# Optimization experiments

Hardware: AMD Instinct MI355X
Metric: run time of the kernel (lower is better)

The kernel has to match this reference:

```python
import jax, jax.numpy as jnp
import numpy as np


def swiglu(g, u):
    return jax.nn.silu(g) * u


def setup_inputs() -> dict:
    key = jax.random.key(0)
    ks = jax.random.split(key, 10)
    D, H, E, HS = 2048, 512, 32, 1024
    B, S = 1, 2048
    s = 0.02
    return {
        "x": jax.random.normal(ks[0], (B, S, D), jnp.float32),
        "gate_w": jax.random.normal(ks[1], (E, D), jnp.float32) * s,
        "expert_bias": jnp.zeros((E,), jnp.float32),
        "wg": jax.random.normal(ks[2], (E, D, H), jnp.float32) * s,
        "wu": jax.random.normal(ks[3], (E, D, H), jnp.float32) * s,
        "wd": jax.random.normal(ks[4], (E, H, D), jnp.float32) * s,
        "sg": jax.random.normal(ks[5], (D, HS), jnp.float32) * s,
        "su": jax.random.normal(ks[6], (D, HS), jnp.float32) * s,
        "sd": jax.random.normal(ks[7], (HS, D), jnp.float32) * s,
        "coef_w": jax.random.normal(ks[8], (2, D), jnp.float32) * s,
        "coef_b": jnp.zeros((2,), jnp.float32),
        "top_k": 4,
    }


def reference(x, gate_w, expert_bias, wg, wu, wd, sg, su, sd, coef_w, coef_b, top_k):
    # --- sigmoid router with bias-adjusted top-k selection ---
    logits = jnp.einsum("bsd,ed->bse", x, gate_w)            # [B,S,E]
    routing = jax.nn.sigmoid(logits.astype(jnp.float32))
    biased = routing + expert_bias[None, None, :]
    _, inds = jax.lax.top_k(biased, top_k)                    # [B,S,k]
    scores = jnp.take_along_axis(routing, inds, axis=-1)      # gather UNbiased weights
    scores = scores / (jnp.sum(scores, axis=-1, keepdims=True) + 1e-20)  # norm_topk_prob
    scores = scores.astype(x.dtype)

    # --- SwitchGLU experts: dense per-expert SwiGLU, then gather top-k outputs ---
    h = jnp.einsum("bsd,edh->bseh", x, wg)                    # [B,S,E,H]
    u = jnp.einsum("bsd,edh->bseh", x, wu)
    y_all = jnp.einsum("bseh,ehd->bsed", swiglu(h, u), wd)    # [B,S,E,D]
    expert_out = jnp.take_along_axis(
        y_all, inds[..., None], axis=2)                        # [B,S,k,D]
    y_experts = jnp.sum(expert_out * scores[..., None], axis=-2)  # [B,S,D]

    # --- shared expert + learned 2-way mixing coefficient ---
    shared = swiglu(x @ sg, x @ su) @ sd                      # [B,S,D]
    coef = jax.nn.softmax(jnp.einsum("bsd,cd->bsc", x, coef_w) + coef_b, axis=-1)
    return y_experts * coef[..., :1] + shared * coef[..., 1:]
```

## Files before the change

kernel.cpp:

```cpp
#include <hip/hip_runtime.h>
#include <hip/hip_bf16.h>
#include <stdint.h>

#define S_TOK   2048
#define DMODEL  2048
#define HEXP    512
#define NEXP    32
#define HSH     1024
#define NPAIR   (S_TOK * 4)
#define NT128   96
#define NT64    160

#define M128_NT  0
#define M128_TE  1
#define M128_TP0 (1 + NT128)
#define M128_TM  (1 + 2 * NT128)
#define M64_NT   (1 + 3 * NT128)
#define M64_TE   (M64_NT + 1)
#define M64_TP0  (M64_NT + 1 + NT64)
#define M64_TM   (M64_NT + 1 + 2 * NT64)
#define META_SIZE (M64_NT + 1 + 3 * NT64)

typedef short  s16x8 __attribute__((ext_vector_type(8)));
typedef __bf16 b16x8 __attribute__((ext_vector_type(8)));
typedef float  f32x4 __attribute__((ext_vector_type(4)));

__device__ __forceinline__ f32x4 mfma16x16x32(s16x8 a, s16x8 b, f32x4 c) {
    return __builtin_amdgcn_mfma_f32_16x16x32_bf16(
        __builtin_bit_cast(b16x8, a), __builtin_bit_cast(b16x8, b), c, 0, 0, 0);
}

__device__ __forceinline__ unsigned short f2bf(float f) {
    union { float f; unsigned int u; } v; v.f = f;
    unsigned int u = v.u;
    return (unsigned short)((u + 0x7FFFu + ((u >> 16) & 1u)) >> 16);
}

__device__ __forceinline__ float bf2f(unsigned short b) {
    union { unsigned int u; float f; } v; v.u = ((unsigned int)b) << 16;
    return v.f;
}

__device__ __forceinline__ void gload16(const unsigned short* g, unsigned short* l) {
    __builtin_amdgcn_global_load_lds(
        (const __attribute__((address_space(1))) void*)(uintptr_t)g,
        (__attribute__((address_space(3))) void*)(uintptr_t)l, 16, 0, 0);
}

__device__ __forceinline__ int src_col8(int lane) {
    return 8 * ((lane & 3) ^ ((lane >> 3) & 3));
}
__device__ __forceinline__ int frag_ko(int fr, int fq) {
    return 8 * (fq ^ ((fr >> 1) & 3));
}

__device__ __forceinline__ void tconv_tile(const float* __restrict__ s,
                                           unsigned short* __restrict__ d,
                                           const int K, const int N,
                                           const int k0, const int n0,
                                           unsigned short* pool)
{
    auto T = (unsigned short (*)[80])pool;
    const int tid = threadIdx.x;
    const int n4 = (tid & 15) * 4;
    const int kr = tid >> 4;
#pragma unroll
    for (int i = 0; i < 4; ++i) {
        const int k = kr + i * 16;
        const float4 v = *reinterpret_cast<const float4*>(s + (size_t)(k0 + k) * N + n0 + n4);
        T[n4 + 0][k] = f2bf(v.x);
        T[n4 + 1][k] = f2bf(v.y);
        T[n4 + 2][k] = f2bf(v.z);
        T[n4 + 3][k] = f2bf(v.w);
    }
    __syncthreads();
    const int nw = tid >> 2;
    const int kc = (tid & 3) * 16;
    uint4* o = reinterpret_cast<uint4*>(d + (size_t)(n0 + nw) * K + k0 + kc);
    o[0] = *reinterpret_cast<const uint4*>(&T[nw][kc]);
    o[1] = *reinterpret_cast<const uint4*>(&T[nw][kc + 8]);
}

__global__ __launch_bounds__(256)
void router_kernel(const float* __restrict__ x, const float* __restrict__ gate_w,
                   const float* __restrict__ expert_bias,
                   const float* __restrict__ coef_w, const float* __restrict__ coef_b,
                   int* __restrict__ inds, float* __restrict__ scores,
                   float* __restrict__ coefo)
{
    const int t = blockIdx.x;
    const int tid = threadIdx.x;
    const int lane = tid & 63;
    const int wave = tid >> 6;
    const float* xr = x + (size_t)t * DMODEL;

    float xv[32];
#pragma unroll
    for (int j = 0; j < 32; ++j) xv[j] = xr[lane + 64 * j];

    __shared__ float s_logits[NEXP];
    __shared__ float s_coef[2];

    for (int i = 0; i < 8; ++i) {
        const int e = wave * 8 + i;
        const float* wr = gate_w + (size_t)e * DMODEL;
        float p = 0.f;
#pragma unroll
        for (int j = 0; j < 32; ++j) p += xv[j] * wr[lane + 64 * j];
#pragma unroll
        for (int o = 32; o > 0; o >>= 1) p += __shfl_xor(p, o);
        if (lane == 0) s_logits[e] = p;
    }
    if (wave == 0) {
        for (int c = 0; c < 2; ++c) {
            const float* wr = coef_w + (size_t)c * DMODEL;
            float p = 0.f;
#pragma unroll
            for (int j = 0; j < 32; ++j) p += xv[j] * wr[lane + 64 * j];
#pragma unroll
            for (int o = 32; o > 0; o >>= 1) p += __shfl_xor(p, o);
            if (lane == 0) s_coef[c] = p;
        }
    }
    __syncthreads();
    if (tid == 0) {
        float routing[NEXP], biased[NEXP];
        for (int e = 0; e < NEXP; ++e) {
            const float r = 1.f / (1.f + expf(-s_logits[e]));
            routing[e] = r;
            biased[e] = r + expert_bias[e];
        }
        int sel[4]; float sc[4]; float ssum = 0.f;
        for (int k = 0; k < 4; ++k) {
            int best = 0; float bv = -1e30f;
            for (int e = 0; e < NEXP; ++e)
                if (biased[e] > bv) { bv = biased[e]; best = e; }
            sel[k] = best; sc[k] = routing[best]; ssum += sc[k];
            biased[best] = -1e30f;
        }
        const float inv = 1.f / (ssum + 1e-20f);
        for (int k = 0; k < 4; ++k) {
            inds[t * 4 + k] = sel[k];
            scores[t * 4 + k] = sc[k] * inv;
        }
        const float l0 = s_coef[0] + coef_b[0];
        const float l1 = s_coef[1] + coef_b[1];
        const float m = fmaxf(l0, l1);
        const float e0 = expf(l0 - m), e1 = expf(l1 - m);
        coefo[t * 2 + 0] = e0 / (e0 + e1);
        coefo[t * 2 + 1] = e1 / (e0 + e1);
    }
}

__global__ __launch_bounds__(256)
void xcast_kernel(const float* __restrict__ x, unsigned short* __restrict__ xb)
{
    const int i = (blockIdx.x * 256 + threadIdx.x) * 4;
    const float4 v = *reinterpret_cast<const float4*>(x + i);
    ushort4 o;
    o.x = f2bf(v.x); o.y = f2bf(v.y); o.z = f2bf(v.z); o.w = f2bf(v.w);
    *reinterpret_cast<ushort4*>(xb + i) = o;
}

__global__ __launch_bounds__(256)
void tconv_kernel(const float* __restrict__ src, unsigned short* __restrict__ dst,
                  const int K, const int N)
{
    __shared__ unsigned short pool[64 * 80];
    const size_t boff = (size_t)blockIdx.z * K * N;
    tconv_tile(src + boff, dst + boff, K, N, blockIdx.y * 64, blockIdx.x * 64, pool);
}

__global__ __launch_bounds__(1024)
void group_kernel(const int* __restrict__ inds, const float* __restrict__ scores,
                  int* __restrict__ meta, int* __restrict__ pair_token,
                  float* __restrict__ pair_score, int* __restrict__ tok_pos)
{
    __shared__ int cnt[NEXP];
    __shared__ int off_s[NEXP];
    __shared__ int cur[NEXP];
    const int tid = threadIdx.x;
    if (tid < NEXP) cnt[tid] = 0;
    __syncthreads();
    for (int i = tid; i < NPAIR; i += 1024) atomicAdd(&cnt[inds[i]], 1);
    __syncthreads();
    if (tid == 0) {
        int run = 0, nt1 = 0, nt2 = 0;
        for (int e = 0; e < NEXP; ++e) {
            off_s[e] = run;
            const int c = cnt[e];
            for (int m0 = 0; m0 < c; m0 += 128) {
                meta[M128_TE + nt1] = e;
                meta[M128_TP0 + nt1] = run + m0;
                meta[M128_TM + nt1] = (c - m0 < 128) ? (c - m0) : 128;
                ++nt1;
            }
            for (int m0 = 0; m0 < c; m0 += 64) {
                meta[M64_TE + nt2] = e;
                meta[M64_TP0 + nt2] = run + m0;
                meta[M64_TM + nt2] = (c - m0 < 64) ? (c - m0) : 64;
                ++nt2;
            }
            run += c;
        }
        meta[M128_NT] = nt1;
        meta[M64_NT] = nt2;
    }
    __syncthreads();
    if (tid < NEXP) cur[tid] = off_s[tid];
    __syncthreads();
    for (int i = tid; i < NPAIR; i += 1024) {
        const int e = inds[i];
        const int pos = atomicAdd(&cur[e], 1);
        pair_token[pos] = i >> 2;
        pair_score[pos] = scores[i];
        tok_pos[i] = pos;
    }
}

__global__ __launch_bounds__(256, 4)
void gateup_e_kernel(const unsigned short* __restrict__ xb,
                     const unsigned short* __restrict__ Bg_all,
                     const unsigned short* __restrict__ Bu_all,
                     unsigned short* __restrict__ act,
                     const int* __restrict__ meta, const int* __restrict__ pair_token,
                     const float* __restrict__ sg, const float* __restrict__ su,
                     const float* __restrict__ sd,
                     unsigned short* __restrict__ sgb, unsigned short* __restrict__ sub_,
                     unsigned short* __restrict__ sdb)
{
    constexpr int NT = DMODEL / 32;
    constexpr int NB = HEXP;
    __shared__ unsigned short pool[16384];
    auto Al  = (unsigned short (*)[128][32])(pool);
    auto Bgl = (unsigned short (*)[64][32])(pool + 8192);
    auto Bul = (unsigned short (*)[64][32])(pool + 12288);

    const int tid = threadIdx.x;
    const int lane = tid & 63;
    const int wave = tid >> 6;

    if (blockIdx.y >= NT128) {
        const int tile = (blockIdx.y - NT128) * 8 + blockIdx.x;
        const int which = tile / 512;
        const int t = tile % 512;
        if (which == 0)      tconv_tile(sg, sgb, DMODEL, HSH, (t >> 4) * 64, (t & 15) * 64, pool);
        else if (which == 1) tconv_tile(su, sub_, DMODEL, HSH, (t >> 4) * 64, (t & 15) * 64, pool);
        else                 tconv_tile(sd, sdb, HSH, DMODEL, (t >> 5) * 64, (t & 31) * 64, pool);
        return;
    }

    const int tt = blockIdx.y;
    if (tt >= meta[M128_NT]) return;
    const int e = meta[M128_TE + tt];
    const int p0 = meta[M128_TP0 + tt];
    const int mval = meta[M128_TM + tt];
    const size_t eoff = (size_t)e * NB * DMODEL;
    const unsigned short* Bg = Bg_all + eoff;
    const unsigned short* Bu = Bu_all + eoff;
    const int n0 = blockIdx.x * 64;

    const int sub  = lane >> 2;
    const int col8 = src_col8(lane);
    const int arow0 = wave * 32 + sub;
    const int arow1 = arow0 + 16;
    int q0 = p0 + arow0; if (q0 > NPAIR - 1) q0 = NPAIR - 1;
    int q1 = p0 + arow1; if (q1 > NPAIR - 1) q1 = NPAIR - 1;
    const int tok0 = pair_token[q0];
    const int tok1 = pair_token[q1];
    const unsigned short* asrc0 = xb + (size_t)tok0 * DMODEL + col8;
    const unsigned short* asrc1 = xb + (size_t)tok1 * DMODEL + col8;
    const int brow = wave * 16 + sub;
    const unsigned short* gsrc = Bg + (size_t)(n0 + brow) * DMODEL + col8;
    const unsigned short* usrc = Bu + (size_t)(n0 + brow) * DMODEL + col8;

    auto stage = [&](int buf, int k0) {
        gload16(asrc0 + k0, &Al[buf][wave * 32][0]);
        gload16(asrc1 + k0, &Al[buf][wave * 32 + 16][0]);
        gload16(gsrc + k0, &Bgl[buf][wave * 16][0]);
        gload16(usrc + k0, &Bul[buf][wave * 16][0]);
    };

    const int wm = wave >> 1, wn = wave & 1;
    const int fr = lane & 15, fq = lane >> 4;
    const int ko = frag_ko(fr, fq);

    const f32x4 zero4 = {0.f, 0.f, 0.f, 0.f};
    f32x4 hacc[4][2], uacc[4][2];
#pragma unroll
    for (int m = 0; m < 4; ++m)
#pragma unroll
        for (int n = 0; n < 2; ++n) { hacc[m][n] = zero4; uacc[m][n] = zero4; }

    auto compute = [&](int buf) {
        s16x8 af[4], bg[2], bu[2];
#pragma unroll
        for (int m = 0; m < 4; ++m)
            af[m] = *reinterpret_cast<const s16x8*>(&Al[buf][wm * 64 + m * 16 + fr][ko]);
#pragma unroll
        for (int n = 0; n < 2; ++n) {
            bg[n] = *reinterpret_cast<const s16x8*>(&Bgl[buf][wn * 32 + n * 16 + fr][ko]);
            bu[n] = *reinterpret_cast<const s16x8*>(&Bul[buf][wn * 32 + n * 16 + fr][ko]);
        }
#pragma unroll
        for (int m = 0; m < 4; ++m)
#pragma unroll
            for (int n = 0; n < 2; ++n) {
                hacc[m][n] = mfma16x16x32(af[m], bg[n], hacc[m][n]);
                uacc[m][n] = mfma16x16x32(af[m], bu[n], uacc[m][n]);
            }
    };

    stage(0, 0);
    __syncthreads();
#pragma unroll 1
    for (int t = 0; t < NT; ++t) {
        const int cur = t & 1;
        if (t + 1 < NT) stage(cur ^ 1, (t + 1) * 32);
        compute(cur);
        __syncthreads();
    }

#pragma unroll
    for (int m = 0; m < 4; ++m)
#pragma unroll
        for (int n = 0; n < 2; ++n) {
            const int col = n0 + wn * 32 + n * 16 + fr;
#pragma unroll
            for (int r = 0; r < 4; ++r) {
                const int rt = wm * 64 + m * 16 + fq * 4 + r;
                if (rt < mval) {
                    const float hv = hacc[m][n][r];
                    const float a = hv / (1.f + __expf(-hv)) * uacc[m][n][r];
                    act[(size_t)(p0 + rt) * NB + col] = f2bf(a);
                }
            }
        }
}

__global__ __launch_bounds__(256, 4)
void gateup_s_kernel(const unsigned short* __restrict__ xb,
                     const unsigned short* __restrict__ Bg,
                     const unsigned short* __restrict__ Bu,
                     unsigned short* __restrict__ act,
                     const float* __restrict__ wd, unsigned short* __restrict__ wdb)
{
    constexpr int NT = DMODEL / 32;
    constexpr int NB = HSH;
    __shared__ unsigned short pool[12288];
    auto Al  = (unsigned short (*)[64][32])(pool);
    auto Bgl = (unsigned short (*)[64][32])(pool + 4096);
    auto Bul = (unsigned short (*)[64][32])(pool + 8192);

    const int tid = threadIdx.x;
    const int lane = tid & 63;
    const int wave = tid >> 6;

    if (blockIdx.y >= S_TOK / 64) {
        const int tile = (blockIdx.y - S_TOK / 64) * 16 + blockIdx.x;
        const int e = tile >> 8;
        const int t = tile & 255;
        tconv_tile(wd + (size_t)e * HEXP * DMODEL, wdb + (size_t)e * DMODEL * HEXP,
                   HEXP, DMODEL, (t >> 5) * 64, (t & 31) * 64, pool);
        return;
    }

    const int p0 = blockIdx.y * 64;
    const int n0 = blockIdx.x * 64;

    const int sub  = lane >> 2;
    const int col8 = src_col8(lane);
    const int arow = wave * 16 + sub;
    const unsigned short* asrc = xb + (size_t)(p0 + arow) * DMODEL + col8;
    const unsigned short* gsrc = Bg + (size_t)(n0 + arow) * DMODEL + col8;
    const unsigned short* usrc = Bu + (size_t)(n0 + arow) * DMODEL + col8;

    auto stage = [&](int buf, int k0) {
        gload16(asrc + k0, &Al[buf][wave * 16][0]);
        gload16(gsrc + k0, &Bgl[buf][wave * 16][0]);
        gload16(usrc + k0, &Bul[buf][wave * 16][0]);
    };

    const int wm = wave >> 1, wn = wave & 1;
    const int fr = lane & 15, fq = lane >> 4;
    const int ko = frag_ko(fr, fq);

    const f32x4 zero4 = {0.f, 0.f, 0.f, 0.f};
    f32x4 hacc[2][2], uacc[2][2];
#pragma unroll
    for (int m = 0; m < 2; ++m)
#pragma unroll
        for (int n = 0; n < 2; ++n) { hacc[m][n] = zero4; uacc[m][n] = zero4; }

    auto compute = [&](int buf) {
        s16x8 af[2], bg[2], bu[2];
#pragma unroll
        for (int m = 0; m < 2; ++m)
            af[m] = *reinterpret_cast<const s16x8*>(&Al[buf][wm * 32 + m * 16 + fr][ko]);
#pragma unroll
        for (int n = 0; n < 2; ++n) {
            bg[n] = *reinterpret_cast<const s16x8*>(&Bgl[buf][wn * 32 + n * 16 + fr][ko]);
            bu[n] = *reinterpret_cast<const s16x8*>(&Bul[buf][wn * 32 + n * 16 + fr][ko]);
        }
#pragma unroll
        for (int m = 0; m < 2; ++m)
#pragma unroll
            for (int n = 0; n < 2; ++n) {
                hacc[m][n] = mfma16x16x32(af[m], bg[n], hacc[m][n]);
                uacc[m][n] = mfma16x16x32(af[m], bu[n], uacc[m][n]);
            }
    };

    stage(0, 0);
    __syncthreads();
#pragma unroll 1
    for (int t = 0; t < NT; ++t) {
        const int cur = t & 1;
        if (t + 1 < NT) stage(cur ^ 1, (t + 1) * 32);
        compute(cur);
        __syncthreads();
    }

#pragma unroll
    for (int m = 0; m < 2; ++m)
#pragma unroll
        for (int n = 0; n < 2; ++n) {
            const int col = n0 + wn * 32 + n * 16 + fr;
#pragma unroll
            for (int r = 0; r < 4; ++r) {
                const int rt = wm * 32 + m * 16 + fq * 4 + r;
                const float hv = hacc[m][n][r];
                const float a = hv / (1.f + __expf(-hv)) * uacc[m][n][r];
                act[(size_t)(p0 + rt) * NB + col] = f2bf(a);
            }
        }
}

template <bool EXPERT, int KA>
__global__ __launch_bounds__(256, 4)
void down_kernel(const unsigned short* __restrict__ act,
                 const unsigned short* __restrict__ Bd_all,
                 float* __restrict__ out, unsigned short* __restrict__ ypair,
                 const int* __restrict__ meta, const int* __restrict__ pair_token,
                 const float* __restrict__ pair_score, const float* __restrict__ coef,
                 const int* __restrict__ tok_pos)
{
    constexpr int NT = KA / 32;
    __shared__ unsigned short Al[2][64][32];
    __shared__ unsigned short Bl[2][64][32];

    const int tid = threadIdx.x;
    const int lane = tid & 63;
    const int wave = tid >> 6;

    int p0, mval;
    const unsigned short* Bd;
    if constexpr (EXPERT) {
        const int tt = blockIdx.y;
        if (tt >= meta[M64_NT]) return;
        const int e = meta[M64_TE + tt];
        p0 = meta[M64_TP0 + tt];
        mval = meta[M64_TM + tt];
        Bd = Bd_all + (size_t)e * DMODEL * KA;
    } else {
        p0 = blockIdx.y * 64;
        mval = 64;
        Bd = Bd_all;
    }
    const int n0 = blockIdx.x * 64;

    const int sub  = lane >> 2;
    const int col8 = src_col8(lane);
    const int arow = wave * 16 + sub;
    int ar = p0 + arow;
    if constexpr (EXPERT) { if (ar > NPAIR - 1) ar = NPAIR - 1; }
    const unsigned short* asrc = act + (size_t)ar * KA + col8;
    const unsigned short* bsrc = Bd + (size_t)(n0 + arow) * KA + col8;

    auto stage = [&](int buf, int k0) {
        gload16(asrc + k0, &Al[buf][wave * 16][0]);
        gload16(bsrc + k0, &Bl[buf][wave * 16][0]);
    };

    const int wm = wave >> 1, wn = wave & 1;
    const int fr = lane & 15, fq = lane >> 4;
    const int ko = frag_ko(fr, fq);

    const f32x4 zero4 = {0.f, 0.f, 0.f, 0.f};
    f32x4 acc[2][2];
#pragma unroll
    for (int m = 0; m < 2; ++m)
#pragma unroll
        for (int n = 0; n < 2; ++n) acc[m][n] = zero4;

    auto compute = [&](int buf) {
        s16x8 af[2], bf[2];
#pragma unroll
        for (int m = 0; m < 2; ++m)
            af[m] = *reinterpret_cast<const s16x8*>(&Al[buf][wm * 32 + m * 16 + fr][ko]);
#pragma unroll
        for (int n = 0; n < 2; ++n)
            bf[n] = *reinterpret_cast<const s16x8*>(&Bl[buf][wn * 32 + n * 16 + fr][ko]);
#pragma unroll
        for (int m = 0; m < 2; ++m)
#pragma unroll
            for (int n = 0; n < 2; ++n)
                acc[m][n] = mfma16x16x32(af[m], bf[n], acc[m][n]);
    };

    stage(0, 0);
    __syncthreads();
#pragma unroll 1
    for (int t = 0; t < NT; ++t) {
        const int cur = t & 1;
        if (t + 1 < NT) stage(cur ^ 1, (t + 1) * 32);
        compute(cur);
        __syncthreads();
    }

#pragma unroll
    for (int m = 0; m < 2; ++m)
#pragma unroll
        for (int n = 0; n < 2; ++n) {
            const int col = n0 + wn * 32 + n * 16 + fr;
#pragma unroll
            for (int r = 0; r < 4; ++r) {
                const int rt = wm * 32 + m * 16 + fq * 4 + r;
                if (rt < mval) {
                    if constexpr (EXPERT) {
                        const int p = p0 + rt;
                        const float s = pair_score[p];
                        ypair[(size_t)p * DMODEL + col] = f2bf(acc[m][n][r] * s);
                    } else {
                        const int row = p0 + rt;
                        float y4 = 0.f;
#pragma unroll
                        for (int k = 0; k < 4; ++k) {
                            const int pos = tok_pos[row * 4 + k];
                            y4 += bf2f(ypair[(size_t)pos * DMODEL + col]);
                        }
                        const float c0 = coef[row * 2 + 0];
                        const float c1 = coef[row * 2 + 1];
                        out[(size_t)row * DMODEL + col] = y4 * c0 + acc[m][n][r] * c1;
                    }
                }
            }
        }
}

extern "C" void kernel_launch(void* const* d_in, const int* in_sizes, int n_in,
                              void* d_out, int out_size, void* d_ws, size_t ws_size,
                              hipStream_t stream)
{
    const float* x           = (const float*)d_in[0];
    const float* gate_w      = (const float*)d_in[1];
    const float* expert_bias = (const float*)d_in[2];
    const float* wg          = (const float*)d_in[3];
    const float* wu          = (const float*)d_in[4];
    const float* wd          = (const float*)d_in[5];
    const float* sg          = (const float*)d_in[6];
    const float* su          = (const float*)d_in[7];
    const float* sd          = (const float*)d_in[8];
    const float* coef_w      = (const float*)d_in[9];
    const float* coef_b      = (const float*)d_in[10];
    float* out = (float*)d_out;

    char* ws = (char*)d_ws;
    size_t off = 0;
    auto take = [&](size_t bytes) {
        char* p = ws + off;
        off = (off + bytes + 255) & ~(size_t)255;
        return p;
    };
    int*   inds     = (int*)  take((size_t)S_TOK * 4 * sizeof(int));
    float* scores   = (float*)take((size_t)S_TOK * 4 * sizeof(float));
    float* coefp    = (float*)take((size_t)S_TOK * 2 * sizeof(float));
    int*   meta     = (int*)  take((size_t)META_SIZE * sizeof(int));
    int*   pair_tok = (int*)  take((size_t)NPAIR * sizeof(int));
    float* pair_sc  = (float*)take((size_t)NPAIR * sizeof(float));
    int*   tok_pos  = (int*)  take((size_t)NPAIR * sizeof(int));
    unsigned short* xb    = (unsigned short*)take((size_t)S_TOK * DMODEL * 2);
    unsigned short* act   = (unsigned short*)take((size_t)NPAIR * HEXP * 2);
    unsigned short* shact = (unsigned short*)take((size_t)S_TOK * HSH * 2);
    unsigned short* ypair = (unsigned short*)take((size_t)NPAIR * DMODEL * 2);
    unsigned short* sgb   = (unsigned short*)take((size_t)HSH * DMODEL * 2);
    unsigned short* sub_  = (unsigned short*)take((size_t)HSH * DMODEL * 2);
    unsigned short* sdb   = (unsigned short*)take((size_t)DMODEL * HSH * 2);
    unsigned short* W1    = (unsigned short*)take((size_t)NEXP * DMODEL * HEXP * 2);
    unsigned short* W2    = (unsigned short*)take((size_t)NEXP * DMODEL * HEXP * 2);
    (void)ws_size; (void)in_sizes; (void)n_in; (void)out_size;

    router_kernel<<<S_TOK, 256, 0, stream>>>(x, gate_w, expert_bias, coef_w, coef_b,
                                             inds, scores, coefp);
    xcast_kernel<<<(S_TOK * DMODEL / 4) / 256, 256, 0, stream>>>(x, xb);
    group_kernel<<<1, 1024, 0, stream>>>(inds, scores, meta, pair_tok, pair_sc, tok_pos);

    tconv_kernel<<<dim3(HEXP / 64, DMODEL / 64, NEXP), 256, 0, stream>>>(wg, W1, DMODEL, HEXP);
    tconv_kernel<<<dim3(HEXP / 64, DMODEL / 64, NEXP), 256, 0, stream>>>(wu, W2, DMODEL, HEXP);

    gateup_e_kernel<<<dim3(HEXP / 64, NT128 + 192), 256, 0, stream>>>(
        xb, W1, W2, act, meta, pair_tok, sg, su, sd, sgb, sub_, sdb);
    gateup_s_kernel<<<dim3(HSH / 64, S_TOK / 64 + 512), 256, 0, stream>>>(
        xb, sgb, sub_, shact, wd, W1);

    down_kernel<true, HEXP><<<dim3(DMODEL / 64, NT64), 256, 0, stream>>>(
        act, W1, out, ypair, meta, pair_tok, pair_sc, nullptr, tok_pos);
    down_kernel<false, HSH><<<dim3(DMODEL / 64, S_TOK / 64), 256, 0, stream>>>(
        shact, sdb, out, ypair, nullptr, nullptr, nullptr, coefp, tok_pos);
}
```

Measured before the change: 362.1 us.

## Merge weight conversions and fuse expert/shared GEMMs into single launches with final combine

Merges all bf16 transpose-conversion work for the gate/up and shared weights into one launch, and adds a separate wd conversion kernel. The expert and shared gate/up GEMMs now run in one flat-grid kernel, as do the expert and shared down GEMMs. A new final kernel gathers the per-pair outputs with vectorised loads and mixes them with the shared result. The transpose tile padding and store width also change. The goal is fewer launches and better load balance across the grid, at the cost of an extra fp32 scratch buffer for the shared down result and one more pass over memory.

Result: no change. 360.5 us (-0.5%).

```diff
diff --git a/kernel.cpp b/kernel.cpp
--- a/kernel.cpp
+++ b/kernel.cpp
@@ -60,7 +60,7 @@
                                            const int k0, const int n0,
                                            unsigned short* pool)
 {
-    auto T = (unsigned short (*)[80])pool;
+    auto T = (unsigned short (*)[84])pool;
     const int tid = threadIdx.x;
     const int n4 = (tid & 15) * 4;
     const int kr = tid >> 4;
@@ -76,9 +76,11 @@
     __syncthreads();
     const int nw = tid >> 2;
     const int kc = (tid & 3) * 16;
-    uint4* o = reinterpret_cast<uint4*>(d + (size_t)(n0 + nw) * K + k0 + kc);
-    o[0] = *reinterpret_cast<const uint4*>(&T[nw][kc]);
-    o[1] = *reinterpret_cast<const uint4*>(&T[nw][kc + 8]);
+    unsigned short* o = d + (size_t)(n0 + nw) * K + k0 + kc;
+#pragma unroll
+    for (int j = 0; j < 4; ++j)
+        *reinterpret_cast<uint2*>(o + j * 4) =
+            *reinterpret_cast<const uint2*>(&T[nw][kc + j * 4]);
 }
 
 __global__ __launch_bounds__(256)
@@ -163,12 +165,42 @@
 }
 
 __global__ __launch_bounds__(256)
-void tconv_kernel(const float* __restrict__ src, unsigned short* __restrict__ dst,
-                  const int K, const int N)
-{
-    __shared__ unsigned short pool[64 * 80];
-    const size_t boff = (size_t)blockIdx.z * K * N;
-    tconv_tile(src + boff, dst + boff, K, N, blockIdx.y * 64, blockIdx.x * 64, pool);
+void tconv_all_kernel(const float* __restrict__ wg, const float* __restrict__ wu,
+                      const float* __restrict__ sg, const float* __restrict__ su,
+                      const float* __restrict__ sd,
+                      unsigned short* __restrict__ W1, unsigned short* __restrict__ W2,
+                      unsigned short* __restrict__ sgb, unsigned short* __restrict__ sub_,
+                      unsigned short* __restrict__ sdb)
+{
+    __shared__ unsigned short pool[64 * 84];
+    const int bid = blockIdx.x;
+    if (bid < 8192) {
+        const int e = bid >> 8, t = bid & 255;
+        tconv_tile(wg + (size_t)e * DMODEL * HEXP, W1 + (size_t)e * HEXP * DMODEL,
+                   DMODEL, HEXP, ((t >> 3) & 31) * 64, (t & 7) * 64, pool);
+    } else if (bid < 16384) {
+        const int e = (bid - 8192) >> 8, t = bid & 255;
+        tconv_tile(wu + (size_t)e * DMODEL * HEXP, W2 + (size_t)e * HEXP * DMODEL,
+                   DMODEL, HEXP, ((t >> 3) & 31) * 64, (t & 7) * 64, pool);
+    } else if (bid < 16896) {
+        const int t = bid - 16384;
+        tconv_tile(sg, sgb, DMODEL, HSH, (t >> 4) * 64, (t & 15) * 64, pool);
+    } else if (bid < 17408) {
+        const int t = bid - 16896;
+        tconv_tile(su, sub_, DMODEL, HSH, (t >> 4) * 64, (t & 15) * 64, pool);
+    } else {
+        const int t = bid - 17408;
+        tconv_tile(sd, sdb, HSH, DMODEL, (t >> 5) * 64, (t & 31) * 64, pool);
+    }
+}
+
+__global__ __launch_bounds__(256)
+void tconv_wd_kernel(const float* __restrict__ wd, unsigned short* __restrict__ wdb)
+{
+    __shared__ unsigned short pool[64 * 84];
+    const int e = blockIdx.x >> 8, t = blockIdx.x & 255;
+    tconv_tile(wd + (size_t)e * HEXP * DMODEL, wdb + (size_t)e * DMODEL * HEXP,
+               HEXP, DMODEL, (t >> 5) * 64, (t & 31) * 64, pool);
 }
 
 __global__ __launch_bounds__(1024)
@@ -219,96 +251,261 @@
 }
 
 __global__ __launch_bounds__(256, 4)
-void gateup_e_kernel(const unsigned short* __restrict__ xb,
-                     const unsigned short* __restrict__ Bg_all,
-                     const unsigned short* __restrict__ Bu_all,
-                     unsigned short* __restrict__ act,
-                     const int* __restrict__ meta, const int* __restrict__ pair_token,
-                     const float* __restrict__ sg, const float* __restrict__ su,
-                     const float* __restrict__ sd,
-                     unsigned short* __restrict__ sgb, unsigned short* __restrict__ sub_,
-                     unsigned short* __restrict__ sdb)
-{
-    constexpr int NT = DMODEL / 32;
-    constexpr int NB = HEXP;
+void gufused_kernel(const unsigned short* __restrict__ xb,
+                    const unsigned short* __restrict__ W1,
+                    const unsigned short* __restrict__ W2,
+                    unsigned short* __restrict__ act,
+                    const int* __restrict__ meta, const int* __restrict__ pair_token,
+                    const unsigned short* __restrict__ sgb,
+                    const unsigned short* __restrict__ sub_,
+                    unsigned short* __restrict__ shact)
+{
     __shared__ unsigned short pool[16384];
-    auto Al  = (unsigned short (*)[128][32])(pool);
-    auto Bgl = (unsigned short (*)[64][32])(pool + 8192);
-    auto Bul = (unsigned short (*)[64][32])(pool + 12288);
-
+    const int bid = blockIdx.x;
     const int tid = threadIdx.x;
     const int lane = tid & 63;
     const int wave = tid >> 6;
-
-    if (blockIdx.y >= NT128) {
-        const int tile = (blockIdx.y - NT128) * 8 + blockIdx.x;
-        const int which = tile / 512;
-        const int t = tile % 512;
-        if (which == 0)      tconv_tile(sg, sgb, DMODEL, HSH, (t >> 4) * 64, (t & 15) * 64, pool);
-        else if (which == 1) tconv_tile(su, sub_, DMODEL, HSH, (t >> 4) * 64, (t & 15) * 64, pool);
-        else                 tconv_tile(sd, sdb, HSH, DMODEL, (t >> 5) * 64, (t & 31) * 64, pool);
-        return;
-    }
-
-    const int tt = blockIdx.y;
-    if (tt >= meta[M128_NT]) return;
-    const int e = meta[M128_TE + tt];
-    const int p0 = meta[M128_TP0 + tt];
-    const int mval = meta[M128_TM + tt];
-    const size_t eoff = (size_t)e * NB * DMODEL;
-    const unsigned short* Bg = Bg_all + eoff;
-    const unsigned short* Bu = Bu_all + eoff;
-    const int n0 = blockIdx.x * 64;
-
-    const int sub  = lane >> 2;
-    const int col8 = src_col8(lane);
-    const int arow0 = wave * 32 + sub;
-    const int arow1 = arow0 + 16;
-    int q0 = p0 + arow0; if (q0 > NPAIR - 1) q0 = NPAIR - 1;
-    int q1 = p0 + arow1; if (q1 > NPAIR - 1) q1 = NPAIR - 1;
-    const int tok0 = pair_token[q0];
-    const int tok1 = pair_token[q1];
-    const unsigned short* asrc0 = xb + (size_t)tok0 * DMODEL + col8;
-    const unsigned short* asrc1 = xb + (size_t)tok1 * DMODEL + col8;
-    const int brow = wave * 16 + sub;
-    const unsigned short* gsrc = Bg + (size_t)(n0 + brow) * DMODEL + col8;
-    const unsigned short* usrc = Bu + (size_t)(n0 + brow) * DMODEL + col8;
-
-    auto stage = [&](int buf, int k0) {
-        gload16(asrc0 + k0, &Al[buf][wave * 32][0]);
-        gload16(asrc1 + k0, &Al[buf][wave * 32 + 16][0]);
-        gload16(gsrc + k0, &Bgl[buf][wave * 16][0]);
-        gload16(usrc + k0, &Bul[buf][wave * 16][0]);
-    };
-
-    const int wm = wave >> 1, wn = wave & 1;
     const int fr = lane & 15, fq = lane >> 4;
     const int ko = frag_ko(fr, fq);
-
+    const int sub = lane >> 2;
+    const int col8 = src_col8(lane);
     const f32x4 zero4 = {0.f, 0.f, 0.f, 0.f};
-    f32x4 hacc[4][2], uacc[4][2];
-#pragma unroll
-    for (int m = 0; m < 4; ++m)
-#pragma unroll
-        for (int n = 0; n < 2; ++n) { hacc[m][n] = zero4; uacc[m][n] = zero4; }
+
+    if (bid < 8 * NT128) {
+        constexpr int NT = DMODEL / 32;
+        constexpr int NB = HEXP;
+        auto Al  = (unsigned short (*)[128][32])(pool);
+        auto Bgl = (unsigned short (*)[64][32])(pool + 8192);
+        auto Bul = (unsigned short (*)[64][32])(pool + 12288);
+
+        const int tt = bid >> 3;
+        if (tt >= meta[M128_NT]) return;
+        const int e = meta[M128_TE + tt];
+        const int p0 = meta[M128_TP0 + tt];
+        const int mval = meta[M128_TM + tt];
+        const size_t eoff = (size_t)e * NB * DMODEL;
+        const unsigned short* Bg = W1 + eoff;
+        const unsigned short* Bu = W2 + eoff;
+        const int n0 = (bid & 7) * 64;
+
+        const int arow0 = wave * 32 + sub;
+        int q0 = p0 + arow0; if (q0 > NPAIR - 1) q0 = NPAIR - 1;
+        int q1 = p0 + arow0 + 16; if (q1 > NPAIR - 1) q1 = NPAIR - 1;
+        const unsigned short* asrc0 = xb + (size_t)pair_token[q0] * DMODEL + col8;
+        const unsigned short* asrc1 = xb + (size_t)pair_token[q1] * DMODEL + col8;
+        const int brow = wave * 16 + sub;
+        const unsigned short* gsrc = Bg + (size_t)(n0 + brow) * DMODEL + col8;
+        const unsigned short* usrc = Bu + (size_t)(n0 + brow) * DMODEL + col8;
+
+        auto stage = [&](int buf, int k0) {
+            gload16(asrc0 + k0, &Al[buf][wave * 32][0]);
+            gload16(asrc1 + k0, &Al[buf][wave * 32 + 16][0]);
+            gload16(gsrc + k0, &Bgl[buf][wave * 16][0]);
+            gload16(usrc + k0, &Bul[buf][wave * 16][0]);
+        };
+
+        const int wm = wave >> 1, wn = wave & 1;
+        f32x4 hacc[4][2], uacc[4][2];
+#pragma unroll
+        for (int m = 0; m < 4; ++m)
+#pragma unroll
+            for (int n = 0; n < 2; ++n) { hacc[m][n] = zero4; uacc[m][n] = zero4; }
+
+        auto compute = [&](int buf) {
+            s16x8 af[4], bg[2], bu[2];
+#pragma unroll
+            for (int m = 0; m < 4; ++m)
+                af[m] = *reinterpret_cast<const s16x8*>(&Al[buf][wm * 64 + m * 16 + fr][ko]);
+#pragma unroll
+            for (int n = 0; n < 2; ++n) {
+                bg[n] = *reinterpret_cast<const s16x8*>(&Bgl[buf][wn * 32 + n * 16 + fr][ko]);
+                bu[n] = *reinterpret_cast<const s16x8*>(&Bul[buf][wn * 32 + n * 16 + fr][ko]);
+            }
+#pragma unroll
+            for (int m = 0; m < 4; ++m)
+#pragma unroll
+                for (int n = 0; n < 2; ++n) {
+                    hacc[m][n] = mfma16x16x32(af[m], bg[n], hacc[m][n]);
+                    uacc[m][n] = mfma16x16x32(af[m], bu[n], uacc[m][n]);
+                }
+        };
+
+        stage(0, 0);
+        __syncthreads();
+#pragma unroll 1
+        for (int t = 0; t < NT; ++t) {
+            const int cur = t & 1;
+            if (t + 1 < NT) stage(cur ^ 1, (t + 1) * 32);
+            compute(cur);
+            __syncthreads();
+        }
+
+#pragma unroll
+        for (int m = 0; m < 4; ++m)
+#pragma unroll
+            for (int n = 0; n < 2; ++n) {
+                const int col = n0 + wn * 32 + n * 16 + fr;
+#pragma unroll
+                for (int r = 0; r < 4; ++r) {
+                    const int rt = wm * 64 + m * 16 + fq * 4 + r;
+                    if (rt < mval) {
+                        const float hv = hacc[m][n][r];
+                        const float a = hv / (1.f + __expf(-hv)) * uacc[m][n][r];
+                        act[(size_t)(p0 + rt) * NB + col] = f2bf(a);
+                    }
+                }
+            }
+    } else {
+        constexpr int NT = DMODEL / 32;
+        constexpr int NB = HSH;
+        auto Al  = (unsigned short (*)[64][32])(pool);
+        auto Bgl = (unsigned short (*)[64][32])(pool + 4096);
+        auto Bul = (unsigned short (*)[64][32])(pool + 8192);
+
+        const int idx = bid - 8 * NT128;
+        const int p0 = (idx >> 4) * 64;
+        const int n0 = (idx & 15) * 64;
+
+        const int arow = wave * 16 + sub;
+        const unsigned short* asrc = xb + (size_t)(p0 + arow) * DMODEL + col8;
+        const unsigned short* gsrc = sgb + (size_t)(n0 + arow) * DMODEL + col8;
+        const unsigned short* usrc = sub_ + (size_t)(n0 + arow) * DMODEL + col8;
+
+        auto stage = [&](int buf, int k0) {
+            gload16(asrc + k0, &Al[buf][wave * 16][0]);
+            gload16(gsrc + k0, &Bgl[buf][wave * 16][0]);
+            gload16(usrc + k0, &Bul[buf][wave * 16][0]);
+        };
+
+        const int wm = wave >> 1, wn = wave & 1;
+        f32x4 hacc[2][2], uacc[2][2];
+#pragma unroll
+        for (int m = 0; m < 2; ++m)
+#pragma unroll
+            for (int n = 0; n < 2; ++n) { hacc[m][n] = zero4; uacc[m][n] = zero4; }
+
+        auto compute = [&](int buf) {
+            s16x8 af[2], bg[2], bu[2];
+#pragma unroll
+            for (int m = 0; m < 2; ++m)
+                af[m] = *reinterpret_cast<const s16x8*>(&Al[buf][wm * 32 + m * 16 + fr][ko]);
+#pragma unroll
+            for (int n = 0; n < 2; ++n) {
+                bg[n] = *reinterpret_cast<const s16x8*>(&Bgl[buf][wn * 32 + n * 16 + fr][ko]);
+                bu[n] = *reinterpret_cast<const s16x8*>(&Bul[buf][wn * 32 + n * 16 + fr][ko]);
+            }
+#pragma unroll
+            for (int m = 0; m < 2; ++m)
+#pragma unroll
+                for (int n = 0; n < 2; ++n) {
+                    hacc[m][n] = mfma16x16x32(af[m], bg[n], hacc[m][n]);
+                    uacc[m][n] = mfma16x16x32(af[m], bu[n], uacc[m][n]);
+                }
+        };
+
+        stage(0, 0);
+        __syncthreads();
+#pragma unroll 1
+        for (int t = 0; t < NT; ++t) {
+            const int cur = t & 1;
+            if (t + 1 < NT) stage(cur ^ 1, (t + 1) * 32);
+            compute(cur);
+            __syncthreads();
+        }
+
+#pragma unroll
+        for (int m = 0; m < 2; ++m)
+#pragma unroll
+            for (int n = 0; n < 2; ++n) {
+                const int col = n0 + wn * 32 + n * 16 + fr;
+#pragma unroll
+                for (int r = 0; r < 4; ++r) {
+                    const int rt = wm * 32 + m * 16 + fq * 4 + r;
+                    const float hv = hacc[m][n][r];
+                    const float a = hv / (1.f + __expf(-hv)) * uacc[m][n][r];
+                    shact[(size_t)(p0 + rt) * NB + col] = f2bf(a);
+                }
+            }
+    }
+}
+
+__global__ __launch_bounds__(256, 4)
+void downfused_kernel(const unsigned short* __restrict__ act,
+                      const unsigned short* __restrict__ shact,
+                      const unsigned short* __restrict__ wdb,
+                      const unsigned short* __restrict__ sdb,
+                      unsigned short* __restrict__ ypair,
+                      float* __restrict__ sdown,
+                      const int* __restrict__ meta,
+                      const float* __restrict__ pair_score)
+{
+    __shared__ unsigned short Al[2][64][32];
+    __shared__ unsigned short Bl[2][64][32];
+    const int bid = blockIdx.x;
+    const int tid = threadIdx.x;
+    const int lane = tid & 63;
+    const int wave = tid >> 6;
+    const int fr = lane & 15, fq = lane >> 4;
+    const int ko = frag_ko(fr, fq);
+    const int sub = lane >> 2;
+    const int col8 = src_col8(lane);
+    const int wm = wave >> 1, wn = wave & 1;
+    const f32x4 zero4 = {0.f, 0.f, 0.f, 0.f};
+
+    const bool EXPERT = bid < 32 * NT64;
+    int p0, mval, n0, KA;
+    const unsigned short *Asrc, *Bd;
+    if (EXPERT) {
+        const int tt = bid >> 5;
+        if (tt >= meta[M64_NT]) return;
+        const int e = meta[M64_TE + tt];
+        p0 = meta[M64_TP0 + tt];
+        mval = meta[M64_TM + tt];
+        n0 = (bid & 31) * 64;
+        KA = HEXP;
+        Asrc = act;
+        Bd = wdb + (size_t)e * DMODEL * HEXP;
+    } else {
+        const int idx = bid - 32 * NT64;
+        p0 = (idx >> 5) * 64;
+        mval = 64;
+        n0 = (idx & 31) * 64;
+        KA = HSH;
+        Asrc = shact;
+        Bd = sdb;
+    }
+    const int NT = KA / 32;
+
+    const int arow = wave * 16 + sub;
+    int ar = p0 + arow;
+    if (EXPERT && ar > NPAIR - 1) ar = NPAIR - 1;
+    const unsigned short* asrc = Asrc + (size_t)ar * KA + col8;
+    const unsigned short* bsrc = Bd + (size_t)(n0 + arow) * KA + col8;
+
+    auto stage = [&](int buf, int k0) {
+        gload16(asrc + k0, &Al[buf][wave * 16][0]);
+        gload16(bsrc + k0, &Bl[buf][wave * 16][0]);
+    };
+
+    f32x4 acc[2][2];
+#pragma unroll
+    for (int m = 0; m < 2; ++m)
+#pragma unroll
+        for (int n = 0; n < 2; ++n) acc[m][n] = zero4;
 
     auto compute = [&](int buf) {
-        s16x8 af[4], bg[2], bu[2];
-#pragma unroll
-        for (int m = 0; m < 4; ++m)
-            af[m] = *reinterpret_cast<const s16x8*>(&Al[buf][wm * 64 + m * 16 + fr][ko]);
-#pragma unroll
-        for (int n = 0; n < 2; ++n) {
-            bg[n] = *reinterpret_cast<const s16x8*>(&Bgl[buf][wn * 32 + n * 16 + fr][ko]);
-            bu[n] = *reinterpret_cast<const s16x8*>(&Bul[buf][wn * 32 + n * 16 + fr][ko]);
-        }
-#pragma unroll
-        for (int m = 0; m < 4; ++m)
-#pragma unroll
-            for (int n = 0; n < 2; ++n) {
-                hacc[m][n] = mfma16x16x32(af[m], bg[n], hacc[m][n]);
-                uacc[m][n] = mfma16x16x32(af[m], bu[n], uacc[m][n]);
-            }
+        s16x8 af[2], bf[2];
+#pragma unroll
+        for (int m = 0; m < 2; ++m)
+            af[m] = *reinterpret_cast<const s16x8*>(&Al[buf][wm * 32 + m * 16 + fr][ko]);
+#pragma unroll
+        for (int n = 0; n < 2; ++n)
+            bf[n] = *reinterpret_cast<const s16x8*>(&Bl[buf][wn * 32 + n * 16 + fr][ko]);
+#pragma unroll
+        for (int m = 0; m < 2; ++m)
+#pragma unroll
+            for (int n = 0; n < 2; ++n)
+                acc[m][n] = mfma16x16x32(af[m], bf[n], acc[m][n]);
     };
 
     stage(0, 0);
@@ -322,203 +519,6 @@
     }
 
 #pragma unroll
-    for (int m = 0; m < 4; ++m)
-#pragma unroll
-        for (int n = 0; n < 2; ++n) {
-            const int col = n0 + wn * 32 + n * 16 + fr;
-#pragma unroll
-            for (int r = 0; r < 4; ++r) {
-                const int rt = wm * 64 + m * 16 + fq * 4 + r;
-                if (rt < mval) {
-                    const float hv = hacc[m][n][r];
-                    const float a = hv / (1.f + __expf(-hv)) * uacc[m][n][r];
-                    act[(size_t)(p0 + rt) * NB + col] = f2bf(a);
-                }
-            }
-        }
-}
-
-__global__ __launch_bounds__(256, 4)
-void gateup_s_kernel(const unsigned short* __restrict__ xb,
-                     const unsigned short* __restrict__ Bg,
-                     const unsigned short* __restrict__ Bu,
-                     unsigned short* __restrict__ act,
-                     const float* __restrict__ wd, unsigned short* __restrict__ wdb)
-{
-    constexpr int NT = DMODEL / 32;
-    constexpr int NB = HSH;
-    __shared__ unsigned short pool[12288];
-    auto Al  = (unsigned short (*)[64][32])(pool);
-    auto Bgl = (unsigned short (*)[64][32])(pool + 4096);
-    auto Bul = (unsigned short (*)[64][32])(pool + 8192);
-
-    const int tid = threadIdx.x;
-    const int lane = tid & 63;
-    const int wave = tid >> 6;
-
-    if (blockIdx.y >= S_TOK / 64) {
-        const int tile = (blockIdx.y - S_TOK / 64) * 16 + blockIdx.x;
-        const int e = tile >> 8;
-        const int t = tile & 255;
-        tconv_tile(wd + (size_t)e * HEXP * DMODEL, wdb + (size_t)e * DMODEL * HEXP,
-                   HEXP, DMODEL, (t >> 5) * 64, (t & 31) * 64, pool);
-        return;
-    }
-
-    const int p0 = blockIdx.y * 64;
-    const int n0 = blockIdx.x * 64;
-
-    const int sub  = lane >> 2;
-    const int col8 = src_col8(lane);
-    const int arow = wave * 16 + sub;
-    const unsigned short* asrc = xb + (size_t)(p0 + arow) * DMODEL + col8;
-    const unsigned short* gsrc = Bg + (size_t)(n0 + arow) * DMODEL + col8;
-    const unsigned short* usrc = Bu + (size_t)(n0 + arow) * DMODEL + col8;
-
-    auto stage = [&](int buf, int k0) {
-        gload16(asrc + k0, &Al[buf][wave * 16][0]);
-        gload16(gsrc + k0, &Bgl[buf][wave * 16][0]);
-        gload16(usrc + k0, &Bul[buf][wave * 16][0]);
-    };
-
-    const int wm = wave >> 1, wn = wave & 1;
-    const int fr = lane & 15, fq = lane >> 4;
-    const int ko = frag_ko(fr, fq);
-
-    const f32x4 zero4 = {0.f, 0.f, 0.f, 0.f};
-    f32x4 hacc[2][2], uacc[2][2];
-#pragma unroll
-    for (int m = 0; m < 2; ++m)
-#pragma unroll
-        for (int n = 0; n < 2; ++n) { hacc[m][n] = zero4; uacc[m][n] = zero4; }
-
-    auto compute = [&](int buf) {
-        s16x8 af[2], bg[2], bu[2];
-#pragma unroll
-        for (int m = 0; m < 2; ++m)
-            af[m] = *reinterpret_cast<const s16x8*>(&Al[buf][wm * 32 + m * 16 + fr][ko]);
-#pragma unroll
-        for (int n = 0; n < 2; ++n) {
-            bg[n] = *reinterpret_cast<const s16x8*>(&Bgl[buf][wn * 32 + n * 16 + fr][ko]);
-            bu[n] = *reinterpret_cast<const s16x8*>(&Bul[buf][wn * 32 + n * 16 + fr][ko]);
-        }
-#pragma unroll
-        for (int m = 0; m < 2; ++m)
-#pragma unroll
-            for (int n = 0; n < 2; ++n) {
-                hacc[m][n] = mfma16x16x32(af[m], bg[n], hacc[m][n]);
-                uacc[m][n] = mfma16x16x32(af[m], bu[n], uacc[m][n]);
-            }
-    };
-
-    stage(0, 0);
-    __syncthreads();
-#pragma unroll 1
-    for (int t = 0; t < NT; ++t) {
-        const int cur = t & 1;
-        if (t + 1 < NT) stage(cur ^ 1, (t + 1) * 32);
-        compute(cur);
-        __syncthreads();
-    }
-
-#pragma unroll
-    for (int m = 0; m < 2; ++m)
-#pragma unroll
-        for (int n = 0; n < 2; ++n) {
-            const int col = n0 + wn * 32 + n * 16 + fr;
-#pragma unroll
-            for (int r = 0; r < 4; ++r) {
-                const int rt = wm * 32 + m * 16 + fq * 4 + r;
-                const float hv = hacc[m][n][r];
-                const float a = hv / (1.f + __expf(-hv)) * uacc[m][n][r];
-                act[(size_t)(p0 + rt) * NB + col] = f2bf(a);
-            }
-        }
-}
-
-template <bool EXPERT, int KA>
-__global__ __launch_bounds__(256, 4)
-void down_kernel(const unsigned short* __restrict__ act,
-                 const unsigned short* __restrict__ Bd_all,
-                 float* __restrict__ out, unsigned short* __restrict__ ypair,
-                 const int* __restrict__ meta, const int* __restrict__ pair_token,
-                 const float* __restrict__ pair_score, const float* __restrict__ coef,
-                 const int* __restrict__ tok_pos)
-{
-    constexpr int NT = KA / 32;
-    __shared__ unsigned short Al[2][64][32];
-    __shared__ unsigned short Bl[2][64][32];
-
-    const int tid = threadIdx.x;
-    const int lane = tid & 63;
-    const int wave = tid >> 6;
-
-    int p0, mval;
-    const unsigned short* Bd;
-    if constexpr (EXPERT) {
-        const int tt = blockIdx.y;
-        if (tt >= meta[M64_NT]) return;
-        const int e = meta[M64_TE + tt];
-        p0 = meta[M64_TP0 + tt];
-        mval = meta[M64_TM + tt];
-        Bd = Bd_all + (size_t)e * DMODEL * KA;
-    } else {
-        p0 = blockIdx.y * 64;
-        mval = 64;
-        Bd = Bd_all;
-    }
-    const int n0 = blockIdx.x * 64;
-
-    const int sub  = lane >> 2;
-    const int col8 = src_col8(lane);
-    const int arow = wave * 16 + sub;
-    int ar = p0 + arow;
-    if constexpr (EXPERT) { if (ar > NPAIR - 1) ar = NPAIR - 1; }
-    const unsigned short* asrc = act + (size_t)ar * KA + col8;
-    const unsigned short* bsrc = Bd + (size_t)(n0 + arow) * KA + col8;
-
-    auto stage = [&](int buf, int k0) {
-        gload16(asrc + k0, &Al[buf][wave * 16][0]);
-        gload16(bsrc + k0, &Bl[buf][wave * 16][0]);
-    };
-
-    const int wm = wave >> 1, wn = wave & 1;
-    const int fr = lane & 15, fq = lane >> 4;
-    const int ko = frag_ko(fr, fq);
-
-    const f32x4 zero4 = {0.f, 0.f, 0.f, 0.f};
-    f32x4 acc[2][2];
-#pragma unroll
-    for (int m = 0; m < 2; ++m)
-#pragma unroll
-        for (int n = 0; n < 2; ++n) acc[m][n] = zero4;
-
-    auto compute = [&](int buf) {
-        s16x8 af[2], bf[2];
-#pragma unroll
-        for (int m = 0; m < 2; ++m)
-            af[m] = *reinterpret_cast<const s16x8*>(&Al[buf][wm * 32 + m * 16 + fr][ko]);
-#pragma unroll
-        for (int n = 0; n < 2; ++n)
-            bf[n] = *reinterpret_cast<const s16x8*>(&Bl[buf][wn * 32 + n * 16 + fr][ko]);
-#pragma unroll
-        for (int m = 0; m < 2; ++m)
-#pragma unroll
-            for (int n = 0; n < 2; ++n)
-                acc[m][n] = mfma16x16x32(af[m], bf[n], acc[m][n]);
-    };
-
-    stage(0, 0);
-    __syncthreads();
-#pragma unroll 1
-    for (int t = 0; t < NT; ++t) {
-        const int cur = t & 1;
-        if (t + 1 < NT) stage(cur ^ 1, (t + 1) * 32);
-        compute(cur);
-        __syncthreads();
-    }
-
-#pragma unroll
     for (int m = 0; m < 2; ++m)
 #pragma unroll
         for (int n = 0; n < 2; ++n) {
@@ -527,25 +527,47 @@
             for (int r = 0; r < 4; ++r) {
                 const int rt = wm * 32 + m * 16 + fq * 4 + r;
                 if (rt < mval) {
-                    if constexpr (EXPERT) {
+                    if (EXPERT) {
                         const int p = p0 + rt;
-                        const float s = pair_score[p];
-                        ypair[(size_t)p * DMODEL + col] = f2bf(acc[m][n][r] * s);
+                        ypair[(size_t)p * DMODEL + col] = f2bf(acc[m][n][r] * pair_score[p]);
                     } else {
-                        const int row = p0 + rt;
-                        float y4 = 0.f;
-#pragma unroll
-                        for (int k = 0; k < 4; ++k) {
-                            const int pos = tok_pos[row * 4 + k];
-                            y4 += bf2f(ypair[(size_t)pos * DMODEL + col]);
-                        }
-                        const float c0 = coef[row * 2 + 0];
-                        const float c1 = coef[row * 2 + 1];
-                        out[(size_t)row * DMODEL + col] = y4 * c0 + acc[m][n][r] * c1;
+                        sdown[(size_t)(p0 + rt) * DMODEL + col] = acc[m][n][r];
                     }
                 }
             }
         }
+}
+
+__global__ __launch_bounds__(256)
+void final_kernel(const unsigned short* __restrict__ ypair,
+                  const float* __restrict__ sdown,
+                  const float* __restrict__ coef, const int* __restrict__ tok_pos,
+                  float* __restrict__ out)
+{
+    const int row = blockIdx.x;
+    const int col = threadIdx.x * 8;
+    float acc[8] = {0.f, 0.f, 0.f, 0.f, 0.f, 0.f, 0.f, 0.f};
+#pragma unroll
+    for (int k = 0; k < 4; ++k) {
+        const int pos = tok_pos[row * 4 + k];
+        const uint4 v = *reinterpret_cast<const uint4*>(ypair + (size_t)pos * DMODEL + col);
+        const unsigned short* u = reinterpret_cast<const unsigned short*>(&v);
+#pragma unroll
+        for (int j = 0; j < 8; ++j) acc[j] += bf2f(u[j]);
+    }
+    const float c0 = coef[row * 2 + 0];
+    const float c1 = coef[row * 2 + 1];
+    const float* sd = sdown + (size_t)row * DMODEL + col;
+    const float4 s0 = *reinterpret_cast<const float4*>(sd);
+    const float4 s1 = *reinterpret_cast<const float4*>(sd + 4);
+    float4 o0, o1;
+    o0.x = acc[0] * c0 + s0.x * c1; o0.y = acc[1] * c0 + s0.y * c1;
+    o0.z = acc[2] * c0 + s0.z * c1; o0.w = acc[3] * c0 + s0.w * c1;
+    o1.x = acc[4] * c0 + s1.x * c1; o1.y = acc[5] * c0 + s1.y * c1;
+    o1.z = acc[6] * c0 + s1.z * c1; o1.w = acc[7] * c0 + s1.w * c1;
+    float* op = out + (size_t)row * DMODEL + col;
+    *reinterpret_cast<float4*>(op) = o0;
+    *reinterpret_cast<float4*>(op + 4) = o1;
 }
 
 extern "C" void kernel_launch(void* const* d_in, const int* in_sizes, int n_in,
@@ -583,6 +605,7 @@
     unsigned short* act   = (unsigned short*)take((size_t)NPAIR * HEXP * 2);
     unsigned short* shact = (unsigned short*)take((size_t)S_TOK * HSH * 2);
     unsigned short* ypair = (unsigned short*)take((size_t)NPAIR * DMODEL * 2);
+    float*          sdown = (float*)take((size_t)S_TOK * DMODEL * 4);
     unsigned short* sgb   = (unsigned short*)take((size_t)HSH * DMODEL * 2);
     unsigned short* sub_  = (unsigned short*)take((size_t)HSH * DMODEL * 2);
     unsigned short* sdb   = (unsigned short*)take((size_t)DMODEL * HSH * 2);
@@ -595,16 +618,16 @@
     xcast_kernel<<<(S_TOK * DMODEL / 4) / 256, 256, 0, stream>>>(x, xb);
     group_kernel<<<1, 1024, 0, stream>>>(inds, scores, meta, pair_tok, pair_sc, tok_pos);
 
-    tconv_kernel<<<dim3(HEXP / 64, DMODEL / 64, NEXP), 256, 0, stream>>>(wg, W1, DMODEL, HEXP);
-    tconv_kernel<<<dim3(HEXP / 64, DMODEL / 64, NEXP), 256, 0, stream>>>(wu, W2, DMODEL, HEXP);
-
-    gateup_e_kernel<<<dim3(HEXP / 64, NT128 + 192), 256, 0, stream>>>(
-        xb, W1, W2, act, meta, pair_tok, sg, su, sd, sgb, sub_, sdb);
-    gateup_s_kernel<<<dim3(HSH / 64, S_TOK / 64 + 512), 256, 0, stream>>>(
-        xb, sgb, sub_, shact, wd, W1);
-
-    down_kernel<true, HEXP><<<dim3(DMODEL / 64, NT64), 256, 0, stream>>>(
-        act, W1, out, ypair, meta, pair_tok, pair_sc, nullptr, tok_pos);
-    down_kernel<false, HSH><<<dim3(DMODEL / 64, S_TOK / 64), 256, 0, stream>>>(
-        shact, sdb, out, ypair, nullptr, nullptr, nullptr, coefp, tok_pos);
-}
+    tconv_all_kernel<<<17920, 256, 0, stream>>>(wg, wu, sg, su, sd,
+                                                W1, W2, sgb, sub_, sdb);
+
+    gufused_kernel<<<8 * NT128 + 512, 256, 0, stream>>>(
+        xb, W1, W2, act, meta, pair_tok, sgb, sub_, shact);
+
+    tconv_wd_kernel<<<NEXP * 256, 256, 0, stream>>>(wd, W1);
+
+    downfused_kernel<<<32 * NT64 + 1024, 256, 0, stream>>>(
+        act, shact, W1, sdb, ypair, sdown, meta, pair_sc);
+
+    final_kernel<<<S_TOK, 256, 0, stream>>>(ypair, sdown, coefp, tok_pos, out);
+}
```
